# Performance work log

Hardware: AMD Instinct MI355X
Metric: run time of the kernel (lower is better)

## Reference

```python
import jax, jax.numpy as jnp
import numpy as np

B, CIN, COUT, H, W = 16, 512, 128, 64, 64


def setup_inputs() -> dict:
    key = jax.random.key(0)
    k1, k2, k3 = jax.random.split(key, 3)
    x = jax.random.normal(k1, (B, CIN, H, W), dtype=jnp.float32)
    style = jax.random.normal(k2, (B, CIN), dtype=jnp.float32)
    # kaiming_normal_ on [COUT, CIN, 1, 1]: fan_in = CIN*1*1, std = sqrt(2/fan_in)
    weight = jax.random.normal(k3, (COUT, CIN), dtype=jnp.float32) * np.float32(np.sqrt(2.0 / CIN))
    return {"x": x, "style": style, "weight": weight}


def reference(x, style, weight):
    # Per-sample modulated weight: mw[b,o,c] = style[b,c] * weight[o,c]
    # 1x1 conv, padding=0, stride=1 -> batched channel-mixing GEMM:
    # out[b,o,h,w] = sum_c mw[b,o,c] * x[b,c,h,w]
    return jnp.einsum('oc,bc,bchw->bohw', weight, style, x)
```

## Files before the change

### kernel.cpp

```cpp
#include <hip/hip_runtime.h>
#include <stdint.h>

#define NB    16
#define CIN   512
#define COUT  128
#define HW    4096
#define BN    128
#define BK    32
#define NIT   (CIN / BK)

using bf16x8  = __attribute__((ext_vector_type(8))) __bf16;
using floatx4 = __attribute__((ext_vector_type(4))) float;

__device__ __forceinline__ unsigned short f2bf_bits(float f) {
    union { float f; unsigned u; } v; v.f = f;
    return (unsigned short)((v.u + 0x7fffu + ((v.u >> 16) & 1u)) >> 16);
}

#define GLD16(g, l)                                                            \
    __builtin_amdgcn_global_load_lds(                                          \
        (const __attribute__((address_space(1))) void*)(g),                    \
        (__attribute__((address_space(3))) void*)(l), 16, 0, 0)

__global__ __launch_bounds__(256)
void modw_kernel(const float* __restrict__ style,
                 const float* __restrict__ weight,
                 __bf16* __restrict__ mw)
{
    const int id = blockIdx.x * 256 + threadIdx.x;
    const int k8 = id & 63;
    const int m  = (id >> 6) & 127;
    const int b  = id >> 13;

    const float4 w0 = *(const float4*)(weight + m * CIN + k8 * 8);
    const float4 w1 = *(const float4*)(weight + m * CIN + k8 * 8 + 4);
    const float4 s0 = *(const float4*)(style + b * CIN + k8 * 8);
    const float4 s1 = *(const float4*)(style + b * CIN + k8 * 8 + 4);

    union { unsigned short us[8]; bf16x8 v; } pk;
    pk.us[0] = f2bf_bits(w0.x * s0.x);
    pk.us[1] = f2bf_bits(w0.y * s0.y);
    pk.us[2] = f2bf_bits(w0.z * s0.z);
    pk.us[3] = f2bf_bits(w0.w * s0.w);
    pk.us[4] = f2bf_bits(w1.x * s1.x);
    pk.us[5] = f2bf_bits(w1.y * s1.y);
    pk.us[6] = f2bf_bits(w1.z * s1.z);
    pk.us[7] = f2bf_bits(w1.w * s1.w);
    *(bf16x8*)(mw + ((size_t)(b * 64 + k8) * 128 + m) * 8) = pk.v;
}

__global__ __launch_bounds__(512, 4)
void modconv1x1_kernel(const float* __restrict__ x,
                       const __bf16* __restrict__ mw,
                       float* __restrict__ out)
{
    __shared__ __align__(16) __bf16 Alds[3][4096];
    __shared__ __align__(16) float  Blds[3][BK * BN];

    const int tid  = threadIdx.x;
    const int lane = tid & 63;
    const int wave = tid >> 6;
    const int quad = lane >> 4;
    const int l15  = lane & 15;

    const int b  = blockIdx.x >> 5;
    const int n0 = (blockIdx.x & 31) * BN;

    const char*  xbb  = (const char*)(x + (size_t)b * CIN * HW + n0);
    float*       outb = out + (size_t)b * COUT * HW + n0;
    const char*  mwb  = (const char*)mw + (size_t)b * (64 * 128 * 16);

    const int wm = (wave & 1) * 64;
    const int wn = (wave >> 1) * 32;

    const int brsel = lane >> 5;
    const int bcol  = lane & 31;

    floatx4 acc[4][2];
    #pragma unroll
    for (int i = 0; i < 4; ++i)
        #pragma unroll
        for (int j = 0; j < 2; ++j)
            acc[i][j] = (floatx4){0.f, 0.f, 0.f, 0.f};

#define STAGE(K0, BUF)                                                         \
    {                                                                          \
        const char* at = mwb + (size_t)(K0) * 256;                             \
        char*       al = (char*)&Alds[BUF][0];                                 \
        GLD16(at + wave * 1024 + lane * 16, al + wave * 1024);                 \
        char* bl = (char*)&Blds[BUF][0];                                       \
        _Pragma("unroll")                                                      \
        for (int g = 0; g < 2; ++g) {                                          \
            const int gi = wave * 2 + g;                            \
            const int r  = gi * 2 + brsel;                      \
            GLD16(xbb + (size_t)((K0) + r) * (HW * 4) + bcol * 16,             \
                  bl + gi * 1024);                                             \
        }                                                                      \
    }

#define COMPUTE(BUF)                                                           \
    {                                                                          \
        bf16x8 af[4];                                                          \
        _Pragma("unroll")                                                      \
        for (int tm = 0; tm < 4; ++tm)                                         \
            af[tm] = *(const bf16x8*)&Alds[BUF][(quad * COUT + wm + tm * 16 + l15) * 8]; \
        bf16x8 bfr[2];                                                         \
        _Pragma("unroll")                                                      \
        for (int tn = 0; tn < 2; ++tn) {                                       \
            union { unsigned short us[8]; bf16x8 v; } pk;                      \
            _Pragma("unroll")                                                  \
            for (int j = 0; j < 8; ++j)                                        \
                pk.us[j] = f2bf_bits(Blds[BUF][(quad * 8 + j) * BN + wn + tn * 16 + l15]); \
            bfr[tn] = pk.v;                                                    \
        }                                                                      \
        _Pragma("unroll")                                                      \
        for (int tm = 0; tm < 4; ++tm)                                         \
            _Pragma("unroll")                                                  \
            for (int tn = 0; tn < 2; ++tn)                                     \
                acc[tm][tn] = __builtin_amdgcn_mfma_f32_16x16x32_bf16(         \
                    af[tm], bfr[tn], acc[tm][tn], 0, 0, 0);                    \
    }

    STAGE(0, 0)
    STAGE(BK, 1)

    int sc = 0;
    int ss = 2;
    int k0 = 2 * BK;
    #pragma unroll 1
    for (int it = 0; it < NIT - 2; ++it) {
        asm volatile("s_waitcnt vmcnt(3)" ::: "memory");
        __builtin_amdgcn_s_barrier();
        STAGE(k0, ss)
        COMPUTE(sc)
        k0 += BK;
        sc = (sc == 2) ? 0 : sc + 1;
        ss = (ss == 2) ? 0 : ss + 1;
    }
    asm volatile("s_waitcnt vmcnt(3)" ::: "memory");
    __builtin_amdgcn_s_barrier();
    COMPUTE(2)
    asm volatile("s_waitcnt vmcnt(0)" ::: "memory");
    __builtin_amdgcn_s_barrier();
    COMPUTE(0)
#undef STAGE
#undef COMPUTE

    #pragma unroll
    for (int tm = 0; tm < 4; ++tm) {
        const int o = wm + tm * 16 + quad * 4;
        #pragma unroll
        for (int tn = 0; tn < 2; ++tn) {
            const int n = wn + tn * 16 + l15;
            #pragma unroll
            for (int r = 0; r < 4; ++r)
                outb[(size_t)(o + r) * HW + n] = acc[tm][tn][r];
        }
    }
}

extern "C" void kernel_launch(void* const* d_in, const int* in_sizes, int n_in,
                              void* d_out, int out_size, void* d_ws, size_t ws_size,
                              hipStream_t stream) {
    const float* x      = (const float*)d_in[0];
    const float* style  = (const float*)d_in[1];
    const float* weight = (const float*)d_in[2];
    float* out = (float*)d_out;
    __bf16* mw = (__bf16*)d_ws;

    modw_kernel<<<dim3(512), dim3(256), 0, stream>>>(style, weight, mw);
    modconv1x1_kernel<<<dim3(NB * 32), dim3(512), 0, stream>>>(x, mw, out);
}
```

Baseline: 209.3 us.

## Fuse style modulation into GEMM by building bf16 A fragments in registers

Result: slower. 234.1 us (+11.8%).

```diff
diff --git a/kernel.cpp b/kernel.cpp
--- a/kernel.cpp
+++ b/kernel.cpp
@@ -22,40 +22,13 @@
         (const __attribute__((address_space(1))) void*)(g),                    \
         (__attribute__((address_space(3))) void*)(l), 16, 0, 0)
 
-__global__ __launch_bounds__(256)
-void modw_kernel(const float* __restrict__ style,
-                 const float* __restrict__ weight,
-                 __bf16* __restrict__ mw)
+__global__ __launch_bounds__(512, 4)
+void modconv_fused_kernel(const float* __restrict__ x,
+                          const float* __restrict__ style,
+                          const float* __restrict__ weight,
+                          float* __restrict__ out)
 {
-    const int id = blockIdx.x * 256 + threadIdx.x;
-    const int k8 = id & 63;
-    const int m  = (id >> 6) & 127;
-    const int b  = id >> 13;
-
-    const float4 w0 = *(const float4*)(weight + m * CIN + k8 * 8);
-    const float4 w1 = *(const float4*)(weight + m * CIN + k8 * 8 + 4);
-    const float4 s0 = *(const float4*)(style + b * CIN + k8 * 8);
-    const float4 s1 = *(const float4*)(style + b * CIN + k8 * 8 + 4);
-
-    union { unsigned short us[8]; bf16x8 v; } pk;
-    pk.us[0] = f2bf_bits(w0.x * s0.x);
-    pk.us[1] = f2bf_bits(w0.y * s0.y);
-    pk.us[2] = f2bf_bits(w0.z * s0.z);
-    pk.us[3] = f2bf_bits(w0.w * s0.w);
-    pk.us[4] = f2bf_bits(w1.x * s1.x);
-    pk.us[5] = f2bf_bits(w1.y * s1.y);
-    pk.us[6] = f2bf_bits(w1.z * s1.z);
-    pk.us[7] = f2bf_bits(w1.w * s1.w);
-    *(bf16x8*)(mw + ((size_t)(b * 64 + k8) * 128 + m) * 8) = pk.v;
-}
-
-__global__ __launch_bounds__(512, 4)
-void modconv1x1_kernel(const float* __restrict__ x,
-                       const __bf16* __restrict__ mw,
-                       float* __restrict__ out)
-{
-    __shared__ __align__(16) __bf16 Alds[3][4096];
-    __shared__ __align__(16) float  Blds[3][BK * BN];
+    __shared__ __align__(16) float Blds[3][BK * BN];
 
     const int tid  = threadIdx.x;
     const int lane = tid & 63;
@@ -68,10 +41,15 @@
 
     const char*  xbb  = (const char*)(x + (size_t)b * CIN * HW + n0);
     float*       outb = out + (size_t)b * COUT * HW + n0;
-    const char*  mwb  = (const char*)mw + (size_t)b * (64 * 128 * 16);
 
     const int wm = (wave & 1) * 64;
     const int wn = (wave >> 1) * 32;
+
+    const float* wr0 = weight + (size_t)(wm + 0 * 16 + l15) * CIN + quad * 8;
+    const float* wr1 = weight + (size_t)(wm + 1 * 16 + l15) * CIN + quad * 8;
+    const float* wr2 = weight + (size_t)(wm + 2 * 16 + l15) * CIN + quad * 8;
+    const float* wr3 = weight + (size_t)(wm + 3 * 16 + l15) * CIN + quad * 8;
+    const float* sb  = style + (size_t)b * CIN + quad * 8;
 
     const int brsel = lane >> 5;
     const int bcol  = lane & 31;
@@ -83,11 +61,8 @@
         for (int j = 0; j < 2; ++j)
             acc[i][j] = (floatx4){0.f, 0.f, 0.f, 0.f};
 
-#define STAGE(K0, BUF)                                                         \
+#define BSTAGE(K0, BUF)                                                        \
     {                                                                          \
-        const char* at = mwb + (size_t)(K0) * 256;                             \
-        char*       al = (char*)&Alds[BUF][0];                                 \
-        GLD16(at + wave * 1024 + lane * 16, al + wave * 1024);                 \
         char* bl = (char*)&Blds[BUF][0];                                       \
         _Pragma("unroll")                                                      \
         for (int g = 0; g < 2; ++g) {                                          \
@@ -98,12 +73,40 @@
         }                                                                      \
     }
 
-#define COMPUTE(BUF)                                                           \
+#define ABUILD(K0, AF)                                                         \
     {                                                                          \
-        bf16x8 af[4];                                                          \
-        _Pragma("unroll")                                                      \
-        for (int tm = 0; tm < 4; ++tm)                                         \
-            af[tm] = *(const bf16x8*)&Alds[BUF][(quad * COUT + wm + tm * 16 + l15) * 8]; \
+        const float4 sv0 = *(const float4*)(sb + (K0));                        \
+        const float4 sv1 = *(const float4*)(sb + (K0) + 4);                    \
+        const float4 w00 = *(const float4*)(wr0 + (K0));                       \
+        const float4 w01 = *(const float4*)(wr0 + (K0) + 4);                   \
+        const float4 w10 = *(const float4*)(wr1 + (K0));                       \
+        const float4 w11 = *(const float4*)(wr1 + (K0) + 4);                   \
+        const float4 w20 = *(const float4*)(wr2 + (K0));                       \
+        const float4 w21 = *(const float4*)(wr2 + (K0) + 4);                   \
+        const float4 w30 = *(const float4*)(wr3 + (K0));                       \
+        const float4 w31 = *(const float4*)(wr3 + (K0) + 4);                   \
+        union { unsigned short us[8]; bf16x8 v; } p0, p1, p2, p3;              \
+        p0.us[0] = f2bf_bits(w00.x * sv0.x); p0.us[1] = f2bf_bits(w00.y * sv0.y); \
+        p0.us[2] = f2bf_bits(w00.z * sv0.z); p0.us[3] = f2bf_bits(w00.w * sv0.w); \
+        p0.us[4] = f2bf_bits(w01.x * sv1.x); p0.us[5] = f2bf_bits(w01.y * sv1.y); \
+        p0.us[6] = f2bf_bits(w01.z * sv1.z); p0.us[7] = f2bf_bits(w01.w * sv1.w); \
+        p1.us[0] = f2bf_bits(w10.x * sv0.x); p1.us[1] = f2bf_bits(w10.y * sv0.y); \
+        p1.us[2] = f2bf_bits(w10.z * sv0.z); p1.us[3] = f2bf_bits(w10.w * sv0.w); \
+        p1.us[4] = f2bf_bits(w11.x * sv1.x); p1.us[5] = f2bf_bits(w11.y * sv1.y); \
+        p1.us[6] = f2bf_bits(w11.z * sv1.z); p1.us[7] = f2bf_bits(w11.w * sv1.w); \
+        p2.us[0] = f2bf_bits(w20.x * sv0.x); p2.us[1] = f2bf_bits(w20.y * sv0.y); \
+        p2.us[2] = f2bf_bits(w20.z * sv0.z); p2.us[3] = f2bf_bits(w20.w * sv0.w); \
+        p2.us[4] = f2bf_bits(w21.x * sv1.x); p2.us[5] = f2bf_bits(w21.y * sv1.y); \
+        p2.us[6] = f2bf_bits(w21.z * sv1.z); p2.us[7] = f2bf_bits(w21.w * sv1.w); \
+        p3.us[0] = f2bf_bits(w30.x * sv0.x); p3.us[1] = f2bf_bits(w30.y * sv0.y); \
+        p3.us[2] = f2bf_bits(w30.z * sv0.z); p3.us[3] = f2bf_bits(w30.w * sv0.w); \
+        p3.us[4] = f2bf_bits(w31.x * sv1.x); p3.us[5] = f2bf_bits(w31.y * sv1.y); \
+        p3.us[6] = f2bf_bits(w31.z * sv1.z); p3.us[7] = f2bf_bits(w31.w * sv1.w); \
+        AF[0] = p0.v; AF[1] = p1.v; AF[2] = p2.v; AF[3] = p3.v;                \
+    }
+
+#define COMPUTE(BUF, AF)                                                       \
+    {                                                                          \
         bf16x8 bfr[2];                                                         \
         _Pragma("unroll")                                                      \
         for (int tn = 0; tn < 2; ++tn) {                                       \
@@ -118,32 +121,34 @@
             _Pragma("unroll")                                                  \
             for (int tn = 0; tn < 2; ++tn)                                     \
                 acc[tm][tn] = __builtin_amdgcn_mfma_f32_16x16x32_bf16(         \
-                    af[tm], bfr[tn], acc[tm][tn], 0, 0, 0);                    \
+                    AF[tm], bfr[tn], acc[tm][tn], 0, 0, 0);                    \
     }
 
-    STAGE(0, 0)
-    STAGE(BK, 1)
+    BSTAGE(0, 0)
+    BSTAGE(BK, 1)
 
     int sc = 0;
     int ss = 2;
-    int k0 = 2 * BK;
     #pragma unroll 1
-    for (int it = 0; it < NIT - 2; ++it) {
-        asm volatile("s_waitcnt vmcnt(3)" ::: "memory");
+    for (int it = 0; it < NIT - 1; ++it) {
+        asm volatile("s_waitcnt vmcnt(2)" ::: "memory");
         __builtin_amdgcn_s_barrier();
-        STAGE(k0, ss)
-        COMPUTE(sc)
-        k0 += BK;
+        bf16x8 af[4];
+        ABUILD(it * BK, af)
+        if (it + 2 < NIT) BSTAGE((it + 2) * BK, ss)
+        COMPUTE(sc, af)
         sc = (sc == 2) ? 0 : sc + 1;
         ss = (ss == 2) ? 0 : ss + 1;
     }
-    asm volatile("s_waitcnt vmcnt(3)" ::: "memory");
-    __builtin_amdgcn_s_barrier();
-    COMPUTE(2)
     asm volatile("s_waitcnt vmcnt(0)" ::: "memory");
     __builtin_amdgcn_s_barrier();
-    COMPUTE(0)
-#undef STAGE
+    {
+        bf16x8 af[4];
+        ABUILD((NIT - 1) * BK, af)
+        COMPUTE(sc, af)
+    }
+#undef BSTAGE
+#undef ABUILD
 #undef COMPUTE
 
     #pragma unroll
@@ -166,8 +171,7 @@
     const float* style  = (const float*)d_in[1];
     const float* weight = (const float*)d_in[2];
     float* out = (float*)d_out;
-    __bf16* mw = (__bf16*)d_ws;
+    (void)d_ws; (void)ws_size;
 
-    modw_kernel<<<dim3(512), dim3(256), 0, stream>>>(style, weight, mw);
-    modconv1x1_kernel<<<dim3(NB * 32), dim3(512), 0, stream>>>(x, mw, out);
+    modconv_fused_kernel<<<dim3(NB * 32), dim3(512), 0, stream>>>(x, style, weight, out);
 }
```

## Convert x tiles to bf16 once in registers before LDS, double-buffer

Applied to the files above, without the earlier changes.

Result: no change. 205.8 us (-1.7%).

```diff
diff --git a/kernel.cpp b/kernel.cpp
--- a/kernel.cpp
+++ b/kernel.cpp
@@ -54,8 +54,8 @@
                        const __bf16* __restrict__ mw,
                        float* __restrict__ out)
 {
-    __shared__ __align__(16) __bf16 Alds[3][4096];
-    __shared__ __align__(16) float  Blds[3][BK * BN];
+    __shared__ __align__(16) __bf16 Alds[2][4096];
+    __shared__ __align__(16) __bf16 Bfs[2][4 * 128 * 8];
 
     const int tid  = threadIdx.x;
     const int lane = tid & 63;
@@ -66,15 +66,15 @@
     const int b  = blockIdx.x >> 5;
     const int n0 = (blockIdx.x & 31) * BN;
 
-    const char*  xbb  = (const char*)(x + (size_t)b * CIN * HW + n0);
     float*       outb = out + (size_t)b * COUT * HW + n0;
     const char*  mwb  = (const char*)mw + (size_t)b * (64 * 128 * 16);
 
     const int wm = (wave & 1) * 64;
     const int wn = (wave >> 1) * 32;
 
-    const int brsel = lane >> 5;
-    const int bcol  = lane & 31;
+    const int kg = tid >> 7;
+    const int bn = tid & 127;
+    const float* xbn = x + (size_t)b * CIN * HW + (size_t)kg * 8 * HW + n0 + bn;
 
     floatx4 acc[4][2];
     #pragma unroll
@@ -83,19 +83,26 @@
         for (int j = 0; j < 2; ++j)
             acc[i][j] = (floatx4){0.f, 0.f, 0.f, 0.f};
 
-#define STAGE(K0, BUF)                                                         \
+#define SISSUE(T, XR)                                                          \
     {                                                                          \
-        const char* at = mwb + (size_t)(K0) * 256;                             \
-        char*       al = (char*)&Alds[BUF][0];                                 \
-        GLD16(at + wave * 1024 + lane * 16, al + wave * 1024);                 \
-        char* bl = (char*)&Blds[BUF][0];                                       \
+        const float* xp = xbn + (size_t)(T) * BK * HW;                         \
         _Pragma("unroll")                                                      \
-        for (int g = 0; g < 2; ++g) {                                          \
-            const int gi = wave * 2 + g;                            \
-            const int r  = gi * 2 + brsel;                      \
-            GLD16(xbb + (size_t)((K0) + r) * (HW * 4) + bcol * 16,             \
-                  bl + gi * 1024);                                             \
-        }                                                                      \
+        for (int j = 0; j < 8; ++j) XR[j] = xp[(size_t)j * HW];                \
+    }
+
+#define SWRITE(T, XR)                                                          \
+    {                                                                          \
+        union { unsigned short us[8]; bf16x8 v; } pk;                          \
+        _Pragma("unroll")                                                      \
+        for (int j = 0; j < 8; ++j) pk.us[j] = f2bf_bits(XR[j]);               \
+        *(bf16x8*)&Bfs[(T) & 1][(kg * 128 + bn) * 8] = pk.v;                   \
+    }
+
+#define ADMA(T)                                                                \
+    {                                                                          \
+        const char* at = mwb + (size_t)(T) * 8192;                             \
+        GLD16(at + wave * 1024 + lane * 16,                                    \
+              (char*)&Alds[(T) & 1][0] + wave * 1024);                        \
     }
 
 #define COMPUTE(BUF)                                                           \
@@ -103,16 +110,11 @@
         bf16x8 af[4];                                                          \
         _Pragma("unroll")                                                      \
         for (int tm = 0; tm < 4; ++tm)                                         \
-            af[tm] = *(const bf16x8*)&Alds[BUF][(quad * COUT + wm + tm * 16 + l15) * 8]; \
+            af[tm] = *(const bf16x8*)&Alds[BUF][(quad * 128 + wm + tm * 16 + l15) * 8]; \
         bf16x8 bfr[2];                                                         \
         _Pragma("unroll")                                                      \
-        for (int tn = 0; tn < 2; ++tn) {                                       \
-            union { unsigned short us[8]; bf16x8 v; } pk;                      \
-            _Pragma("unroll")                                                  \
-            for (int j = 0; j < 8; ++j)                                        \
-                pk.us[j] = f2bf_bits(Blds[BUF][(quad * 8 + j) * BN + wn + tn * 16 + l15]); \
-            bfr[tn] = pk.v;                                                    \
-        }                                                                      \
+        for (int tn = 0; tn < 2; ++tn)                                         \
+            bfr[tn] = *(const bf16x8*)&Bfs[BUF][(quad * 128 + wn + tn * 16 + l15) * 8]; \
         _Pragma("unroll")                                                      \
         for (int tm = 0; tm < 4; ++tm)                                         \
             _Pragma("unroll")                                                  \
@@ -121,30 +123,45 @@
                     af[tm], bfr[tn], acc[tm][tn], 0, 0, 0);                    \
     }
 
-    STAGE(0, 0)
-    STAGE(BK, 1)
+#define BODYF(IT, XC, XN)                                                      \
+    {                                                                          \
+        ADMA((IT) + 1)                                                         \
+        COMPUTE((IT) & 1)                                                      \
+        SISSUE((IT) + 2, XN)                                                   \
+        SWRITE((IT) + 1, XC)                                                   \
+        asm volatile("s_waitcnt vmcnt(8) lgkmcnt(0)" ::: "memory");            \
+        __builtin_amdgcn_s_barrier();                                          \
+    }
 
-    int sc = 0;
-    int ss = 2;
-    int k0 = 2 * BK;
+    float xa[8], xb[8];
+
+    SISSUE(0, xa)
+    ADMA(0)
+    SWRITE(0, xa)
+    SISSUE(1, xb)
+    asm volatile("s_waitcnt vmcnt(8) lgkmcnt(0)" ::: "memory");
+    __builtin_amdgcn_s_barrier();
+
     #pragma unroll 1
-    for (int it = 0; it < NIT - 2; ++it) {
-        asm volatile("s_waitcnt vmcnt(3)" ::: "memory");
+    for (int it2 = 0; it2 < 7; ++it2) {
+        const int it = it2 * 2;
+        BODYF(it,     xb, xa)
+        BODYF(it + 1, xa, xb)
+    }
+    {
+        ADMA(15)
+        COMPUTE(0)
+        SWRITE(15, xb)
+        asm volatile("s_waitcnt vmcnt(0) lgkmcnt(0)" ::: "memory");
         __builtin_amdgcn_s_barrier();
-        STAGE(k0, ss)
-        COMPUTE(sc)
-        k0 += BK;
-        sc = (sc == 2) ? 0 : sc + 1;
-        ss = (ss == 2) ? 0 : ss + 1;
     }
-    asm volatile("s_waitcnt vmcnt(3)" ::: "memory");
-    __builtin_amdgcn_s_barrier();
-    COMPUTE(2)
-    asm volatile("s_waitcnt vmcnt(0)" ::: "memory");
-    __builtin_amdgcn_s_barrier();
-    COMPUTE(0)
-#undef STAGE
+    COMPUTE(1)
+
+#undef BODYF
 #undef COMPUTE
+#undef ADMA
+#undef SWRITE
+#undef SISSUE
 
     #pragma unroll
     for (int tm = 0; tm < 4; ++tm) {
```
